# Performance work log

Measured on AMD Instinct MI355X. Metric: run time of the kernel, lower is better.

Reference implementation:

```python
import jax, jax.numpy as jnp
import numpy as np

N = 100000          # num nodes
E = 1_600_000       # num edges
D = 128             # in_channels
H = 128             # hidden_channels
NUM_LAYERS = 3


def setup_inputs() -> dict:
    key = jax.random.key(0)
    ks = jax.random.split(key, 6)
    return {
        "emb": jax.random.normal(ks[0], (N, D), dtype=jnp.float32),
        "w1": jax.random.normal(ks[1], (H, D), dtype=jnp.float32) / np.sqrt(D).astype(np.float32),
        "b1": jnp.zeros((H,), jnp.float32),
        "w2": jax.random.normal(ks[2], (H, H), dtype=jnp.float32) / np.sqrt(H).astype(np.float32),
        "b2": jnp.zeros((H,), jnp.float32),
        "eps": jnp.zeros((NUM_LAYERS,), jnp.float32),  # learn_eps=True, init 0 per layer
        "edge_w": jax.random.uniform(ks[3], (E,), dtype=jnp.float32),
        "src": jax.random.randint(ks[4], (E,), 0, N, dtype=jnp.int32),
        "dst": jax.random.randint(ks[5], (E,), 0, N, dtype=jnp.int32),
    }


def _gin_layer(x, src, dst, edge_w, deg_inv, eps, W, b):
    # DGL GINConv(mean, edge_weight): msg = x[src] * w ; agg = mean over in-edges (divide by in-degree)
    msg = x[src] * edge_w[:, None]                                  # [E, d]
    agg = jax.ops.segment_sum(msg, dst, num_segments=N) * deg_inv[:, None]
    return ((1.0 + eps) * x + agg) @ W.T + b


def reference(emb, w1, b1, w2, b2, eps, edge_w, src, dst):
    # in-degree (count of in-edges), zero-degree nodes get 0 aggregation
    deg = jax.ops.segment_sum(jnp.ones((E,), jnp.float32), dst, num_segments=N)
    deg_inv = jnp.where(deg > 0, 1.0 / jnp.maximum(deg, 1.0), 0.0)

    x = _gin_layer(emb, src, dst, edge_w, deg_inv, eps[0], w1, b1)
    x = jax.nn.relu(x)  # dropout is identity in eval mode
    for i in range(1, NUM_LAYERS - 1):
        x = _gin_layer(x, src, dst, edge_w, deg_inv, eps[i], w2, b2)  # lin2 shared
        x = jax.nn.relu(x)
    x = _gin_layer(x, src, dst, edge_w, deg_inv, eps[NUM_LAYERS - 1], w2, b2)
    x = x.at[0].set(jnp.zeros((x.shape[1],), x.dtype))  # x[0] = zeros
    return x
```

## Files before the change

### kernel.cpp

```cpp
#include <hip/hip_runtime.h>
#include <hip/hip_bf16.h>

#define N_NODES 100000
#define N_EDGES 1600000
#define DIM 128
#define SCAN_CHUNK 1024

typedef __attribute__((ext_vector_type(8))) short bf16x8;
typedef __attribute__((ext_vector_type(4))) float f32x4;
typedef __attribute__((ext_vector_type(4))) short bf16x4;

__global__ void cvtall_kernel(const float* __restrict__ emb, const float* __restrict__ w1,
                              const float* __restrict__ w2, __hip_bfloat16* __restrict__ embb,
                              __hip_bfloat16* __restrict__ w1b, __hip_bfloat16* __restrict__ w2b) {
    const int n4e = N_NODES * DIM / 4;
    const int n4w = DIM * DIM / 4;
    int i = blockIdx.x * blockDim.x + threadIdx.x;
    const float* in;
    __hip_bfloat16* out;
    int j;
    if (i < n4e) { in = emb; out = embb; j = i; }
    else if (i < n4e + n4w) { in = w1; out = w1b; j = i - n4e; }
    else if (i < n4e + 2 * n4w) { in = w2; out = w2b; j = i - n4e - n4w; }
    else return;
    f32x4 v = ((const f32x4*)in)[j];
    bf16x4 o;
    o.x = (short)__bfloat16_as_ushort(__float2bfloat16(v.x));
    o.y = (short)__bfloat16_as_ushort(__float2bfloat16(v.y));
    o.z = (short)__bfloat16_as_ushort(__float2bfloat16(v.z));
    o.w = (short)__bfloat16_as_ushort(__float2bfloat16(v.w));
    ((bf16x4*)out)[j] = o;
}

__global__ void degrank_kernel(const int* __restrict__ dst, int* __restrict__ deg,
                               int* __restrict__ rank) {
    for (int e = blockIdx.x * blockDim.x + threadIdx.x; e < N_EDGES; e += gridDim.x * blockDim.x)
        rank[e] = atomicAdd(&deg[dst[e]], 1);
}

__global__ void scan1_kernel(const int* __restrict__ deg, int* __restrict__ bsum) {
    __shared__ int s[256];
    int t = threadIdx.x;
    int base = blockIdx.x * SCAN_CHUNK + t * 4;
    int v = 0;
    for (int k = 0; k < 4; k++) { int i = base + k; if (i < N_NODES) v += deg[i]; }
    s[t] = v;
    __syncthreads();
    for (int off = 128; off > 0; off >>= 1) { if (t < off) s[t] += s[t + off]; __syncthreads(); }
    if (t == 0) bsum[blockIdx.x] = s[0];
}

__global__ void scan2_kernel(const int* __restrict__ bsum, int* __restrict__ bscan,
                             int* __restrict__ row_start, int nb) {
    if (threadIdx.x == 0) {
        int run = 0;
        for (int b = 0; b < nb; b++) { bscan[b] = run; run += bsum[b]; }
        row_start[N_NODES] = run;
    }
}

__global__ void scan3_kernel(const int* __restrict__ deg, const int* __restrict__ bscan,
                             int* __restrict__ row_start) {
    __shared__ int s[256];
    int t = threadIdx.x;
    int base = blockIdx.x * SCAN_CHUNK + t * 4;
    int v[4]; int tot = 0;
    for (int k = 0; k < 4; k++) { int i = base + k; v[k] = (i < N_NODES) ? deg[i] : 0; tot += v[k]; }
    s[t] = tot;
    __syncthreads();
    for (int off = 1; off < 256; off <<= 1) {
        int a = (t >= off) ? s[t - off] : 0;
        __syncthreads();
        s[t] += a;
        __syncthreads();
    }
    int run = s[t] - tot + bscan[blockIdx.x];
    for (int k = 0; k < 4; k++) {
        int i = base + k;
        if (i < N_NODES) row_start[i] = run;
        run += v[k];
    }
}

#define FI_UNROLL 4
__global__ void fill_kernel(const int* __restrict__ src, const int* __restrict__ dst,
                            const float* __restrict__ ew, const int* __restrict__ rank,
                            const int* __restrict__ row_start, int2* __restrict__ sw_s) {
    int tid = blockIdx.x * blockDim.x + threadIdx.x;
    int nthreads = gridDim.x * blockDim.x;
    int d_[FI_UNROLL], r_[FI_UNROLL], s_[FI_UNROLL], w_[FI_UNROLL], rs_[FI_UNROLL];
#pragma unroll
    for (int k = 0; k < FI_UNROLL; k++) {
        int e = tid + k * nthreads;
        if (e < N_EDGES) {
            d_[k] = dst[e]; r_[k] = rank[e]; s_[k] = src[e]; w_[k] = __float_as_int(ew[e]);
        } else d_[k] = -1;
    }
#pragma unroll
    for (int k = 0; k < FI_UNROLL; k++)
        if (d_[k] >= 0) rs_[k] = row_start[d_[k]];
#pragma unroll
    for (int k = 0; k < FI_UNROLL; k++)
        if (d_[k] >= 0) sw_s[rs_[k] + r_[k]] = make_int2(s_[k], w_[k]);
}

template <int RELU, int ZERO0, int OUTBF>
__global__ __launch_bounds__(256) void aggmm_kernel(const __hip_bfloat16* __restrict__ x,
                                                    const int* __restrict__ row_start,
                                                    const int2* __restrict__ sw_s,
                                                    const float* __restrict__ eps, int li,
                                                    const __hip_bfloat16* __restrict__ W,
                                                    const float* __restrict__ bias,
                                                    void* __restrict__ outv) {
    __shared__ int2 s_sw[4][64];
    __shared__ __hip_bfloat162 s_h[16][64];
    int wv = threadIdx.x >> 6;
    int lane = threadIdx.x & 63;
    int row0 = blockIdx.x * 16;
    const __hip_bfloat162* xp = (const __hip_bfloat162*)x;
    float ep = 1.0f + eps[li];

    for (int jj = 0; jj < 4; jj++) {
        int j = wv * 4 + jj;
        int n = row0 + j;
        __hip_bfloat162 o;
        o.x = __float2bfloat16(0.f);
        o.y = __float2bfloat16(0.f);
        if (n < N_NODES) {
            int beg = row_start[n], end = row_start[n + 1];
            float ax = 0.f, ay = 0.f;
            for (int base = beg; base < end; base += 64) {
                int cnt = min(64, end - base);
                if (lane < cnt) s_sw[wv][lane] = sw_s[base + lane];
                asm volatile("s_waitcnt lgkmcnt(0)" ::: "memory");
                int i = 0;
                for (; i + 4 <= cnt; i += 4) {
                    int2 e0 = s_sw[wv][i], e1 = s_sw[wv][i + 1];
                    int2 e2 = s_sw[wv][i + 2], e3 = s_sw[wv][i + 3];
                    __hip_bfloat162 v0 = xp[(size_t)e0.x * 64 + lane];
                    __hip_bfloat162 v1 = xp[(size_t)e1.x * 64 + lane];
                    __hip_bfloat162 v2 = xp[(size_t)e2.x * 64 + lane];
                    __hip_bfloat162 v3 = xp[(size_t)e3.x * 64 + lane];
                    float w0 = __int_as_float(e0.y), w1 = __int_as_float(e1.y);
                    float w2 = __int_as_float(e2.y), w3 = __int_as_float(e3.y);
                    ax += __bfloat162float(v0.x) * w0 + __bfloat162float(v1.x) * w1
                        + __bfloat162float(v2.x) * w2 + __bfloat162float(v3.x) * w3;
                    ay += __bfloat162float(v0.y) * w0 + __bfloat162float(v1.y) * w1
                        + __bfloat162float(v2.y) * w2 + __bfloat162float(v3.y) * w3;
                }
                for (; i < cnt; i++) {
                    int2 e = s_sw[wv][i];
                    __hip_bfloat162 v = xp[(size_t)e.x * 64 + lane];
                    float w = __int_as_float(e.y);
                    ax += __bfloat162float(v.x) * w;
                    ay += __bfloat162float(v.y) * w;
                }
                asm volatile("" ::: "memory");
            }
            int degn = end - beg;
            float dinv = degn > 0 ? 1.0f / (float)degn : 0.0f;
            __hip_bfloat162 xs = xp[(size_t)n * 64 + lane];
            o.x = __float2bfloat16(ep * __bfloat162float(xs.x) + ax * dinv);
            o.y = __float2bfloat16(ep * __bfloat162float(xs.y) + ay * dinv);
        }
        int co = (lane * 4) ^ ((j & 7) << 4);
        *(__hip_bfloat162*)((char*)&s_h[j][0] + co) = o;
    }
    __syncthreads();

    int lr = lane & 15;
    int kg = lane >> 4;
    bf16x8 a[4];
#pragma unroll
    for (int k = 0; k < 4; k++) {
        int cb = (kg * 16 + k * 64) ^ ((lr & 7) << 4);
        a[k] = *(const bf16x8*)((const char*)&s_h[lr][0] + cb);
    }

    f32x4 acc[2];
#pragma unroll
    for (int t = 0; t < 2; t++) {
        int jt = wv * 2 + t;
        const short* Wp = (const short*)W + (size_t)(jt * 16 + lr) * DIM + kg * 8;
        f32x4 c = {0.f, 0.f, 0.f, 0.f};
#pragma unroll
        for (int k = 0; k < 4; k++) {
            bf16x8 b = *(const bf16x8*)(Wp + k * 32);
            c = __builtin_amdgcn_mfma_f32_16x16x32_bf16(a[k], b, c, 0, 0, 0);
        }
        acc[t] = c;
    }

    int colb = lane & 15;
    int rb = (lane >> 4) * 4;
#pragma unroll
    for (int t = 0; t < 2; t++) {
        int col = (wv * 2 + t) * 16 + colb;
        float bv = bias[col];
#pragma unroll
        for (int r = 0; r < 4; r++) {
            int grow = row0 + rb + r;
            if (grow < N_NODES) {
                float v = acc[t][r] + bv;
                if (RELU) v = fmaxf(v, 0.f);
                if (ZERO0 && grow == 0) v = 0.f;
                if (OUTBF)
                    ((__hip_bfloat16*)outv)[(size_t)grow * DIM + col] = __float2bfloat16(v);
                else
                    ((float*)outv)[(size_t)grow * DIM + col] = v;
            }
        }
    }
}

extern "C" void kernel_launch(void* const* d_in, const int* in_sizes, int n_in,
                              void* d_out, int out_size, void* d_ws, size_t ws_size,
                              hipStream_t stream) {
    const float* emb = (const float*)d_in[0];
    const float* w1  = (const float*)d_in[1];
    const float* b1  = (const float*)d_in[2];
    const float* w2  = (const float*)d_in[3];
    const float* b2  = (const float*)d_in[4];
    const float* eps = (const float*)d_in[5];
    const float* ew  = (const float*)d_in[6];
    const int* src   = (const int*)d_in[7];
    const int* dst   = (const int*)d_in[8];
    float* out = (float*)d_out;

    char* base = (char*)d_ws;
    size_t off = 0;
    auto alloc = [&](size_t bytes) -> char* {
        char* p = base + off;
        off += (bytes + 255) & ~(size_t)255;
        return p;
    };
    int* deg            = (int*)alloc((size_t)N_NODES * 4);
    int* row_start      = (int*)alloc((size_t)(N_NODES + 1) * 4);
    int* rank           = (int*)alloc((size_t)N_EDGES * 4);
    int* bsum           = (int*)alloc(128 * 4);
    int* bscan          = (int*)alloc(128 * 4);
    int2* sw_s          = (int2*)alloc((size_t)N_EDGES * 8);
    __hip_bfloat16* xb  = (__hip_bfloat16*)alloc((size_t)N_NODES * DIM * 2);
    __hip_bfloat16* xc  = (__hip_bfloat16*)alloc((size_t)N_NODES * DIM * 2);
    __hip_bfloat16* embb= (__hip_bfloat16*)alloc((size_t)N_NODES * DIM * 2);
    __hip_bfloat16* w1b = (__hip_bfloat16*)alloc(DIM * DIM * 2);
    __hip_bfloat16* w2b = (__hip_bfloat16*)alloc(DIM * DIM * 2);

    hipMemsetAsync(deg, 0, (size_t)N_NODES * 4, stream);

    {
        int n4 = N_NODES * DIM / 4 + 2 * (DIM * DIM / 4);
        cvtall_kernel<<<(n4 + 255) / 256, 256, 0, stream>>>(emb, w1, w2, embb, w1b, w2b);
    }

    degrank_kernel<<<2048, 256, 0, stream>>>(dst, deg, rank);
    int nb = (N_NODES + SCAN_CHUNK - 1) / SCAN_CHUNK;
    scan1_kernel<<<nb, 256, 0, stream>>>(deg, bsum);
    scan2_kernel<<<1, 64, 0, stream>>>(bsum, bscan, row_start, nb);
    scan3_kernel<<<nb, 256, 0, stream>>>(deg, bscan, row_start);
    {
        int nthreads = ((N_EDGES + FI_UNROLL - 1) / FI_UNROLL + 255) & ~255;
        fill_kernel<<<nthreads / 256, 256, 0, stream>>>(src, dst, ew, rank, row_start, sw_s);
    }

    int blocks = (N_NODES + 15) / 16;
    aggmm_kernel<1, 0, 1><<<blocks, 256, 0, stream>>>(embb, row_start, sw_s, eps, 0, w1b, b1, xb);
    aggmm_kernel<1, 0, 1><<<blocks, 256, 0, stream>>>(xb,   row_start, sw_s, eps, 1, w2b, b2, xc);
    aggmm_kernel<0, 1, 0><<<blocks, 256, 0, stream>>>(xc,   row_start, sw_s, eps, 2, w2b, b2, out);
}
```

Before: 521.1 us.

## Split neighbor gather across half-waves with 8-byte loads and staged bf16 stores

The aggregation gather now has each half-wave handle alternate edges, with every lane loading 4 bf16 values (8 bytes) through a pre-shifted source byte offset. The two halves are then combined with a cross-half shuffle. The bf16 epilogue stages results through shared memory so each row is written with 16-byte coalesced stores. The degree/rank kernel is unrolled into four independent atomics per thread, and the N-bounds checks are dropped on the assumption that N is divisible by 16. This is meant to raise memory-level parallelism and cut load/store instruction count, in exchange for hardcoded sizes and an extra barrier.

```diff
diff --git a/kernel.cpp b/kernel.cpp
--- a/kernel.cpp
+++ b/kernel.cpp
@@ -9,6 +9,10 @@
 typedef __attribute__((ext_vector_type(8))) short bf16x8;
 typedef __attribute__((ext_vector_type(4))) float f32x4;
 typedef __attribute__((ext_vector_type(4))) short bf16x4;
+
+__device__ __forceinline__ float b2f(short s) {
+    return __uint_as_float(((unsigned int)(unsigned short)s) << 16);
+}
 
 __global__ void cvtall_kernel(const float* __restrict__ emb, const float* __restrict__ w1,
                               const float* __restrict__ w2, __hip_bfloat16* __restrict__ embb,
@@ -32,10 +36,24 @@
     ((bf16x4*)out)[j] = o;
 }
 
-__global__ void degrank_kernel(const int* __restrict__ dst, int* __restrict__ deg,
-                               int* __restrict__ rank) {
-    for (int e = blockIdx.x * blockDim.x + threadIdx.x; e < N_EDGES; e += gridDim.x * blockDim.x)
-        rank[e] = atomicAdd(&deg[dst[e]], 1);
+__global__ __launch_bounds__(256) void degrank_kernel(const int* __restrict__ dst,
+                                                      int* __restrict__ deg,
+                                                      int* __restrict__ rank) {
+    const int S = 2048 * 256;
+    int tid = blockIdx.x * blockDim.x + threadIdx.x;
+    int e3 = tid + 3 * S;
+    int d0 = dst[tid];
+    int d1 = dst[tid + S];
+    int d2 = dst[tid + 2 * S];
+    int d3 = (e3 < N_EDGES) ? dst[e3] : -1;
+    int r0 = atomicAdd(&deg[d0], 1);
+    int r1 = atomicAdd(&deg[d1], 1);
+    int r2 = atomicAdd(&deg[d2], 1);
+    int r3 = (d3 >= 0) ? atomicAdd(&deg[d3], 1) : 0;
+    rank[tid] = r0;
+    rank[tid + S] = r1;
+    rank[tid + 2 * S] = r2;
+    if (e3 < N_EDGES) rank[e3] = r3;
 }
 
 __global__ void scan1_kernel(const int* __restrict__ deg, int* __restrict__ bsum) {
@@ -93,7 +111,7 @@
     for (int k = 0; k < FI_UNROLL; k++) {
         int e = tid + k * nthreads;
         if (e < N_EDGES) {
-            d_[k] = dst[e]; r_[k] = rank[e]; s_[k] = src[e]; w_[k] = __float_as_int(ew[e]);
+            d_[k] = dst[e]; r_[k] = rank[e]; s_[k] = src[e] << 8; w_[k] = __float_as_int(ew[e]);
         } else d_[k] = -1;
     }
 #pragma unroll
@@ -112,59 +130,66 @@
                                                     const __hip_bfloat16* __restrict__ W,
                                                     const float* __restrict__ bias,
                                                     void* __restrict__ outv) {
-    __shared__ int2 s_sw[4][64];
+    __shared__ int2 s_sw[4][66];
     __shared__ __hip_bfloat162 s_h[16][64];
     int wv = threadIdx.x >> 6;
     int lane = threadIdx.x & 63;
     int row0 = blockIdx.x * 16;
-    const __hip_bfloat162* xp = (const __hip_bfloat162*)x;
+    int c = lane & 31;
+    int half = lane >> 5;
+    const char* xb = (const char*)x + (c << 3);
     float ep = 1.0f + eps[li];
 
     for (int jj = 0; jj < 4; jj++) {
         int j = wv * 4 + jj;
         int n = row0 + j;
-        __hip_bfloat162 o;
-        o.x = __float2bfloat16(0.f);
-        o.y = __float2bfloat16(0.f);
-        if (n < N_NODES) {
-            int beg = row_start[n], end = row_start[n + 1];
-            float ax = 0.f, ay = 0.f;
-            for (int base = beg; base < end; base += 64) {
-                int cnt = min(64, end - base);
-                if (lane < cnt) s_sw[wv][lane] = sw_s[base + lane];
-                asm volatile("s_waitcnt lgkmcnt(0)" ::: "memory");
-                int i = 0;
-                for (; i + 4 <= cnt; i += 4) {
-                    int2 e0 = s_sw[wv][i], e1 = s_sw[wv][i + 1];
-                    int2 e2 = s_sw[wv][i + 2], e3 = s_sw[wv][i + 3];
-                    __hip_bfloat162 v0 = xp[(size_t)e0.x * 64 + lane];
-                    __hip_bfloat162 v1 = xp[(size_t)e1.x * 64 + lane];
-                    __hip_bfloat162 v2 = xp[(size_t)e2.x * 64 + lane];
-                    __hip_bfloat162 v3 = xp[(size_t)e3.x * 64 + lane];
-                    float w0 = __int_as_float(e0.y), w1 = __int_as_float(e1.y);
-                    float w2 = __int_as_float(e2.y), w3 = __int_as_float(e3.y);
-                    ax += __bfloat162float(v0.x) * w0 + __bfloat162float(v1.x) * w1
-                        + __bfloat162float(v2.x) * w2 + __bfloat162float(v3.x) * w3;
-                    ay += __bfloat162float(v0.y) * w0 + __bfloat162float(v1.y) * w1
-                        + __bfloat162float(v2.y) * w2 + __bfloat162float(v3.y) * w3;
-                }
-                for (; i < cnt; i++) {
-                    int2 e = s_sw[wv][i];
-                    __hip_bfloat162 v = xp[(size_t)e.x * 64 + lane];
-                    float w = __int_as_float(e.y);
-                    ax += __bfloat162float(v.x) * w;
-                    ay += __bfloat162float(v.y) * w;
-                }
-                asm volatile("" ::: "memory");
+        int beg = row_start[n], end = row_start[n + 1];
+        float a0 = 0.f, a1 = 0.f, a2 = 0.f, a3 = 0.f;
+        for (int base = beg; base < end; base += 64) {
+            int cnt = min(64, end - base);
+            if (lane < cnt) s_sw[wv][lane] = sw_s[base + lane];
+            else if (lane == cnt) s_sw[wv][lane] = make_int2(0, 0);
+            asm volatile("s_waitcnt lgkmcnt(0)" ::: "memory");
+            int cnt2 = (cnt + 1) & ~1;
+            int i = 0;
+            for (; i + 4 <= cnt2; i += 4) {
+                int2 ea = s_sw[wv][i + half];
+                int2 eb = s_sw[wv][i + 2 + half];
+                bf16x4 va = *(const bf16x4*)(xb + ea.x);
+                bf16x4 vb = *(const bf16x4*)(xb + eb.x);
+                float wa = __int_as_float(ea.y), wb = __int_as_float(eb.y);
+                a0 += b2f(va.x) * wa + b2f(vb.x) * wb;
+                a1 += b2f(va.y) * wa + b2f(vb.y) * wb;
+                a2 += b2f(va.z) * wa + b2f(vb.z) * wb;
+                a3 += b2f(va.w) * wa + b2f(vb.w) * wb;
             }
+            for (; i < cnt2; i += 2) {
+                int2 e = s_sw[wv][i + half];
+                bf16x4 v = *(const bf16x4*)(xb + e.x);
+                float w = __int_as_float(e.y);
+                a0 += b2f(v.x) * w;
+                a1 += b2f(v.y) * w;
+                a2 += b2f(v.z) * w;
+                a3 += b2f(v.w) * w;
+            }
+            asm volatile("" ::: "memory");
+        }
+        a0 += __shfl_xor(a0, 32, 64);
+        a1 += __shfl_xor(a1, 32, 64);
+        a2 += __shfl_xor(a2, 32, 64);
+        a3 += __shfl_xor(a3, 32, 64);
+        if (half == 0) {
             int degn = end - beg;
             float dinv = degn > 0 ? 1.0f / (float)degn : 0.0f;
-            __hip_bfloat162 xs = xp[(size_t)n * 64 + lane];
-            o.x = __float2bfloat16(ep * __bfloat162float(xs.x) + ax * dinv);
-            o.y = __float2bfloat16(ep * __bfloat162float(xs.y) + ay * dinv);
-        }
-        int co = (lane * 4) ^ ((j & 7) << 4);
-        *(__hip_bfloat162*)((char*)&s_h[j][0] + co) = o;
+            bf16x4 xs = *(const bf16x4*)((const char*)x + (size_t)n * 256 + (c << 3));
+            bf16x4 o;
+            o.x = (short)__bfloat16_as_ushort(__float2bfloat16(ep * b2f(xs.x) + a0 * dinv));
+            o.y = (short)__bfloat16_as_ushort(__float2bfloat16(ep * b2f(xs.y) + a1 * dinv));
+            o.z = (short)__bfloat16_as_ushort(__float2bfloat16(ep * b2f(xs.z) + a2 * dinv));
+            o.w = (short)__bfloat16_as_ushort(__float2bfloat16(ep * b2f(xs.w) + a3 * dinv));
+            int co = (c * 8) ^ ((j & 7) << 4);
+            *(bf16x4*)((char*)&s_h[j][0] + co) = o;
+        }
     }
     __syncthreads();
 
@@ -176,38 +201,56 @@
         int cb = (kg * 16 + k * 64) ^ ((lr & 7) << 4);
         a[k] = *(const bf16x8*)((const char*)&s_h[lr][0] + cb);
     }
+    __syncthreads();
 
     f32x4 acc[2];
 #pragma unroll
     for (int t = 0; t < 2; t++) {
         int jt = wv * 2 + t;
         const short* Wp = (const short*)W + (size_t)(jt * 16 + lr) * DIM + kg * 8;
-        f32x4 c = {0.f, 0.f, 0.f, 0.f};
+        f32x4 cc = {0.f, 0.f, 0.f, 0.f};
 #pragma unroll
         for (int k = 0; k < 4; k++) {
             bf16x8 b = *(const bf16x8*)(Wp + k * 32);
-            c = __builtin_amdgcn_mfma_f32_16x16x32_bf16(a[k], b, c, 0, 0, 0);
-        }
-        acc[t] = c;
+            cc = __builtin_amdgcn_mfma_f32_16x16x32_bf16(a[k], b, cc, 0, 0, 0);
+        }
+        acc[t] = cc;
     }
 
     int colb = lane & 15;
     int rb = (lane >> 4) * 4;
-#pragma unroll
-    for (int t = 0; t < 2; t++) {
-        int col = (wv * 2 + t) * 16 + colb;
-        float bv = bias[col];
-#pragma unroll
-        for (int r = 0; r < 4; r++) {
-            int grow = row0 + rb + r;
-            if (grow < N_NODES) {
+    if (OUTBF) {
+#pragma unroll
+        for (int t = 0; t < 2; t++) {
+            int col = (wv * 2 + t) * 16 + colb;
+            float bv = bias[col];
+#pragma unroll
+            for (int r = 0; r < 4; r++) {
+                int row = rb + r;
+                float v = acc[t][r] + bv;
+                if (RELU) v = fmaxf(v, 0.f);
+                if (ZERO0 && blockIdx.x == 0 && row == 0) v = 0.f;
+                int bo = (row * 256 + col * 2) ^ ((row & 7) << 4);
+                *(__hip_bfloat16*)((char*)s_h + bo) = __float2bfloat16(v);
+            }
+        }
+        __syncthreads();
+        int row = threadIdx.x >> 4, c16 = threadIdx.x & 15;
+        int bo = (row * 256 + c16 * 16) ^ ((row & 7) << 4);
+        bf16x8 vv = *(const bf16x8*)((const char*)s_h + bo);
+        *(bf16x8*)((char*)outv + (size_t)(row0 + row) * 256 + c16 * 16) = vv;
+    } else {
+#pragma unroll
+        for (int t = 0; t < 2; t++) {
+            int col = (wv * 2 + t) * 16 + colb;
+            float bv = bias[col];
+#pragma unroll
+            for (int r = 0; r < 4; r++) {
+                int grow = row0 + rb + r;
                 float v = acc[t][r] + bv;
                 if (RELU) v = fmaxf(v, 0.f);
                 if (ZERO0 && grow == 0) v = 0.f;
-                if (OUTBF)
-                    ((__hip_bfloat16*)outv)[(size_t)grow * DIM + col] = __float2bfloat16(v);
-                else
-                    ((float*)outv)[(size_t)grow * DIM + col] = v;
+                ((float*)outv)[(size_t)grow * DIM + col] = v;
             }
         }
     }
@@ -263,7 +306,7 @@
         fill_kernel<<<nthreads / 256, 256, 0, stream>>>(src, dst, ew, rank, row_start, sw_s);
     }
 
-    int blocks = (N_NODES + 15) / 16;
+    int blocks = N_NODES / 16;
     aggmm_kernel<1, 0, 1><<<blocks, 256, 0, stream>>>(embb, row_start, sw_s, eps, 0, w1b, b1, xb);
     aggmm_kernel<1, 0, 1><<<blocks, 256, 0, stream>>>(xb,   row_start, sw_s, eps, 1, w2b, b2, xc);
     aggmm_kernel<0, 1, 0><<<blocks, 256, 0, stream>>>(xc,   row_start, sw_s, eps, 2, w2b, b2, out);
```

Measured after the change: 498.0 us. -4.4%, faster.
